# Kernel optimization log

Hardware: AMD Instinct MI355X
Metric: run time of the kernel (lower is better)

Reference implementation:

```python
import jax, jax.numpy as jnp
import numpy as np

H = 1536          # hidden_size
NUM_HEADS = 12
NUM_KV = 2
HEAD_DIM = 128
GQA_REP = NUM_HEADS // NUM_KV  # 6
MAX_CACHE = 131072
SCALE = HEAD_DIM ** -0.5


def setup_inputs() -> dict:
    key = jax.random.key(0)
    ks = jax.random.split(key, 8)
    w = 0.02  # weight init scale for numerical sanity
    return {
        "hidden_states": jax.random.normal(ks[0], (1, H, 1, 1), dtype=jnp.float32),
        "Wq": jax.random.normal(ks[1], (NUM_HEADS * HEAD_DIM, H), dtype=jnp.float32) * w,
        "Wk": jax.random.normal(ks[2], (NUM_KV * HEAD_DIM, H), dtype=jnp.float32) * w,
        "Wv": jax.random.normal(ks[3], (NUM_KV * HEAD_DIM, H), dtype=jnp.float32) * w,
        "Wo": jax.random.normal(ks[4], (H, NUM_HEADS * HEAD_DIM), dtype=jnp.float32) * w,
        "kv_cache_k": jax.random.normal(ks[5], (1, NUM_KV, MAX_CACHE, HEAD_DIM), dtype=jnp.float32),
        "kv_cache_v": jax.random.normal(ks[6], (1, NUM_KV, MAX_CACHE, HEAD_DIM), dtype=jnp.float32),
        "pos": MAX_CACHE - 1,  # python int: current cache write position
    }


def reference(hidden_states, Wq, Wk, Wv, Wo, kv_cache_k, kv_cache_v, pos):
    # 1x1 Conv2d on a [1,H,1,1] tensor == matvec.
    x = hidden_states.reshape(H)                      # [H]
    q = (Wq @ x).reshape(NUM_KV, GQA_REP, HEAD_DIM)   # [g, r, d]
    k = (Wk @ x).reshape(NUM_KV, 1, HEAD_DIM)         # [g, 1, d]
    v = (Wv @ x).reshape(NUM_KV, 1, HEAD_DIM)
    # in-place cache write at pos (pos < MAX_CACHE in this setup)
    kc = jax.lax.dynamic_update_slice(kv_cache_k[0], k, (0, pos, 0))  # [g, L, d]
    vc = jax.lax.dynamic_update_slice(kv_cache_v[0], v, (0, pos, 0))
    seq_len = min(pos + 1, MAX_CACHE)  # pos is a python int -> static slice
    kc = kc[:, :seq_len, :]
    vc = vc[:, :seq_len, :]
    # GQA without materializing repeated K/V: fold repeat into the q head axis.
    scores = jnp.einsum('grd,gld->grl', q, kc) * SCALE       # [g, r, L]
    attn = jax.nn.softmax(scores, axis=-1)
    out = jnp.einsum('grl,gld->grd', attn, vc)               # [g, r, d]
    y = Wo @ out.reshape(NUM_HEADS * HEAD_DIM)               # [H]
    return y.reshape(1, H, 1, 1)
```

## Files before the change

kernel.cpp:

```cpp
#include <hip/hip_runtime.h>
#include <math.h>

#define HDIM 1536
#define NUM_HEADS 12
#define NUM_KV 2
#define HEAD_DIM 128
#define GQA_REP 6
#define MAX_CACHE 131072
#define SCALE 0.08838834764831845f

#define WS_Q    0
#define WS_OUT  2048
#define WS_L2   4096
#define WS_PART 65536
#define REC 132

#define UNITS_PER_G 1024
#define NEG_BIG (-1.0e30f)
#define MASK_NEG (-1.0e38f)

__global__ __launch_bounds__(256) void proj_qkv(
    const float* __restrict__ x, const float* __restrict__ Wq,
    const float* __restrict__ Wk, const float* __restrict__ Wv,
    float* __restrict__ kv_k, float* __restrict__ kv_v,
    const int* __restrict__ pos_p, float* __restrict__ ws)
{
    int r    = (blockIdx.x * 256 + threadIdx.x) >> 6;
    int lane = threadIdx.x & 63;

    const float* Wrow;
    if (r < HDIM)            Wrow = Wq + (size_t)r * HDIM;
    else if (r < HDIM + 256) Wrow = Wk + (size_t)(r - HDIM) * HDIM;
    else                     Wrow = Wv + (size_t)(r - HDIM - 256) * HDIM;

    const float4* w4 = (const float4*)Wrow;
    const float4* x4 = (const float4*)x;
    float sum = 0.f;
#pragma unroll
    for (int it = 0; it < 6; ++it) {
        float4 a = w4[lane + 64 * it];
        float4 b = x4[lane + 64 * it];
        sum += a.x * b.x + a.y * b.y + a.z * b.z + a.w * b.w;
    }
#pragma unroll
    for (int off = 32; off >= 1; off >>= 1) sum += __shfl_xor(sum, off);

    if (lane == 0) {
        if (r < HDIM) {
            ws[WS_Q + r] = sum * SCALE;
        } else {
            int pos = *pos_p;
            if (r < HDIM + 256) {
                int j = r - HDIM; int g = j >> 7, d = j & 127;
                kv_k[((size_t)g * MAX_CACHE + pos) * HEAD_DIM + d] = sum;
            } else {
                int j = r - HDIM - 256; int g = j >> 7, d = j & 127;
                kv_v[((size_t)g * MAX_CACHE + pos) * HEAD_DIM + d] = sum;
            }
        }
    }
}

__global__ __launch_bounds__(256, 4) void attn_decode(
    const float* __restrict__ kv_k, const float* __restrict__ kv_v,
    const int* __restrict__ pos_p, float* __restrict__ ws)
{
    __shared__ float lds[4][GQA_REP][REC];

    int b    = blockIdx.x;
    int g    = b >> 10;
    int ublk = b & 1023;
    int wid  = threadIdx.x >> 6;
    int lane = threadIdx.x & 63;
    int h    = lane >> 5;
    int j    = lane & 31;

    int seq_len = *pos_p + 1;
    if (seq_len > MAX_CACHE) seq_len = MAX_CACHE;

    const float* qb = ws + WS_Q + g * (GQA_REP * HEAD_DIM);
    float4 q[GQA_REP];
#pragma unroll
    for (int r = 0; r < GQA_REP; ++r)
        q[r] = ((const float4*)(qb + r * HEAD_DIM))[j];

    float  m[GQA_REP], l[GQA_REP];
    float4 acc[GQA_REP];
#pragma unroll
    for (int r = 0; r < GQA_REP; ++r) {
        m[r] = NEG_BIG; l[r] = 0.f;
        acc[r].x = acc[r].y = acc[r].z = acc[r].w = 0.f;
    }

    int wbase = ublk * 128 + wid * 32;
    const float4* Kp = (const float4*)(kv_k + ((size_t)g * MAX_CACHE + wbase) * HEAD_DIM);
    const float4* Vp = (const float4*)(kv_v + ((size_t)g * MAX_CACHE + wbase) * HEAD_DIM);
    int i0 = h * 32 + j;

    float4 KA = Kp[i0],      KB = Kp[i0 + 64];
    float4 VA = Vp[i0],      VB = Vp[i0 + 64];

    for (int t = 0; t < 8; ++t) {
        float4 KAn, KBn, VAn, VBn;
        if (t < 7) {
            int n = i0 + (t + 1) * 128;
            KAn = Kp[n]; KBn = Kp[n + 64];
            VAn = Vp[n]; VBn = Vp[n + 64];
        }
        int pA = wbase + 4 * t + h;
        float maskA = (pA     < seq_len) ? 0.f : MASK_NEG;
        float maskB = (pA + 2 < seq_len) ? 0.f : MASK_NEG;

#pragma unroll
        for (int r = 0; r < GQA_REP; ++r) {
            float sA = KA.x * q[r].x + KA.y * q[r].y + KA.z * q[r].z + KA.w * q[r].w;
            float sB = KB.x * q[r].x + KB.y * q[r].y + KB.z * q[r].z + KB.w * q[r].w;
#pragma unroll
            for (int off = 16; off >= 1; off >>= 1) {
                sA += __shfl_xor(sA, off);
                sB += __shfl_xor(sB, off);
            }
            sA += maskA; sB += maskB;

            float mn    = fmaxf(m[r], fmaxf(sA, sB));
            float alpha = __expf(m[r] - mn);
            float pa    = __expf(sA - mn);
            float pb    = __expf(sB - mn);
            l[r] = l[r] * alpha + pa + pb;
            acc[r].x = acc[r].x * alpha + pa * VA.x + pb * VB.x;
            acc[r].y = acc[r].y * alpha + pa * VA.y + pb * VB.y;
            acc[r].z = acc[r].z * alpha + pa * VA.z + pb * VB.z;
            acc[r].w = acc[r].w * alpha + pa * VA.w + pb * VB.w;
            m[r] = mn;
        }
        KA = KAn; KB = KBn; VA = VAn; VB = VBn;
    }

#pragma unroll
    for (int r = 0; r < GQA_REP; ++r) {
        float mo = __shfl_xor(m[r], 32);
        float lo = __shfl_xor(l[r], 32);
        float4 ao;
        ao.x = __shfl_xor(acc[r].x, 32);
        ao.y = __shfl_xor(acc[r].y, 32);
        ao.z = __shfl_xor(acc[r].z, 32);
        ao.w = __shfl_xor(acc[r].w, 32);
        float M  = fmaxf(m[r], mo);
        float a0 = __expf(m[r] - M);
        float a1 = __expf(mo   - M);
        float L  = l[r] * a0 + lo * a1;
        float4 A;
        A.x = acc[r].x * a0 + ao.x * a1;
        A.y = acc[r].y * a0 + ao.y * a1;
        A.z = acc[r].z * a0 + ao.z * a1;
        A.w = acc[r].w * a0 + ao.w * a1;

        if (lane < 32) ((float4*)&lds[wid][r][4])[j] = A;
        if (lane == 0) { lds[wid][r][0] = M; lds[wid][r][1] = L; }
    }
    __syncthreads();

    for (int r = wid; r < GQA_REP; r += 4) {
        float m0 = lds[0][r][0], m1 = lds[1][r][0];
        float m2 = lds[2][r][0], m3 = lds[3][r][0];
        float M = fmaxf(fmaxf(m0, m1), fmaxf(m2, m3));
        float w0 = __expf(m0 - M), w1 = __expf(m1 - M);
        float w2 = __expf(m2 - M), w3 = __expf(m3 - M);
        float L = lds[0][r][1] * w0 + lds[1][r][1] * w1
                + lds[2][r][1] * w2 + lds[3][r][1] * w3;

        float2 a0v = ((const float2*)&lds[0][r][4])[lane];
        float2 a1v = ((const float2*)&lds[1][r][4])[lane];
        float2 a2v = ((const float2*)&lds[2][r][4])[lane];
        float2 a3v = ((const float2*)&lds[3][r][4])[lane];
        float2 a;
        a.x = a0v.x * w0 + a1v.x * w1 + a2v.x * w2 + a3v.x * w3;
        a.y = a0v.y * w0 + a1v.y * w1 + a2v.y * w2 + a3v.y * w3;

        float* rec = ws + WS_PART + ((size_t)(g * UNITS_PER_G + ublk) * GQA_REP + r) * REC;
        ((float2*)(rec + 4))[lane] = a;
        if (lane == 0) { rec[0] = M; rec[1] = L; }
    }
}

__global__ __launch_bounds__(64) void combine1(float* __restrict__ ws)
{
    int b  = blockIdx.x;
    int hh = b >> 5;
    int s  = b & 31;
    int g = hh / GQA_REP, r = hh % GQA_REP;
    int t  = threadIdx.x;
    int um = t & 31;

    const float* base = ws + WS_PART +
        ((size_t)(g * UNITS_PER_G + s * 32) * GQA_REP + r) * REC;
    const float* rec = base + (size_t)um * GQA_REP * REC;
    float mu = rec[0], lu = rec[1];

    float M = mu;
#pragma unroll
    for (int off = 16; off >= 1; off >>= 1) M = fmaxf(M, __shfl_xor(M, off));
    float w = __expf(mu - M);
    float L = lu * w;
#pragma unroll
    for (int off = 16; off >= 1; off >>= 1) L += __shfl_xor(L, off);

    float2 a; a.x = 0.f; a.y = 0.f;
    for (int uu = 0; uu < 32; ++uu) {
        float wu = __shfl(w, uu);
        float2 av = ((const float2*)(base + (size_t)uu * GQA_REP * REC + 4))[t];
        a.x += wu * av.x;
        a.y += wu * av.y;
    }
    float* orec = ws + WS_L2 + (size_t)(hh * 32 + s) * REC;
    ((float2*)(orec + 4))[t] = a;
    if (t == 0) { orec[0] = M; orec[1] = L; }
}

__global__ __launch_bounds__(64) void combine2(float* __restrict__ ws)
{
    int hh = blockIdx.x;
    int t  = threadIdx.x;
    int um = t & 31;

    const float* base = ws + WS_L2 + (size_t)(hh * 32) * REC;
    const float* rec  = base + (size_t)um * REC;
    float mu = rec[0], lu = rec[1];

    float M = mu;
#pragma unroll
    for (int off = 16; off >= 1; off >>= 1) M = fmaxf(M, __shfl_xor(M, off));
    float w = __expf(mu - M);
    float L = lu * w;
#pragma unroll
    for (int off = 16; off >= 1; off >>= 1) L += __shfl_xor(L, off);

    float2 a; a.x = 0.f; a.y = 0.f;
    for (int uu = 0; uu < 32; ++uu) {
        float wu = __shfl(w, uu);
        float2 av = ((const float2*)(base + (size_t)uu * REC + 4))[t];
        a.x += wu * av.x;
        a.y += wu * av.y;
    }
    float invL = 1.f / L;
    ws[WS_OUT + hh * HEAD_DIM + 2 * t]     = a.x * invL;
    ws[WS_OUT + hh * HEAD_DIM + 2 * t + 1] = a.y * invL;
}

__global__ __launch_bounds__(256) void proj_out(
    const float* __restrict__ Wo, const float* __restrict__ ws,
    float* __restrict__ y)
{
    int r    = (blockIdx.x * 256 + threadIdx.x) >> 6;
    int lane = threadIdx.x & 63;
    const float4* w4 = (const float4*)(Wo + (size_t)r * HDIM);
    const float4* o4 = (const float4*)(ws + WS_OUT);
    float sum = 0.f;
#pragma unroll
    for (int it = 0; it < 6; ++it) {
        float4 a = w4[lane + 64 * it];
        float4 b = o4[lane + 64 * it];
        sum += a.x * b.x + a.y * b.y + a.z * b.z + a.w * b.w;
    }
#pragma unroll
    for (int off = 32; off >= 1; off >>= 1) sum += __shfl_xor(sum, off);
    if (lane == 0) y[r] = sum;
}

extern "C" void kernel_launch(void* const* d_in, const int* in_sizes, int n_in,
                              void* d_out, int out_size, void* d_ws, size_t ws_size,
                              hipStream_t stream) {
    const float* x   = (const float*)d_in[0];
    const float* Wq  = (const float*)d_in[1];
    const float* Wk  = (const float*)d_in[2];
    const float* Wv  = (const float*)d_in[3];
    const float* Wo  = (const float*)d_in[4];
    float*       kvk = (float*)d_in[5];
    float*       kvv = (float*)d_in[6];
    const int*   pos = (const int*)d_in[7];
    float* ws = (float*)d_ws;
    float* y  = (float*)d_out;

    proj_qkv   <<<512,  256, 0, stream>>>(x, Wq, Wk, Wv, kvk, kvv, pos, ws);
    attn_decode<<<2048, 256, 0, stream>>>(kvk, kvv, pos, ws);
    combine1   <<<384,   64, 0, stream>>>(ws);
    combine2   <<< 12,   64, 0, stream>>>(ws);
    proj_out   <<<384,  256, 0, stream>>>(Wo, ws, y);
}
```

Measured before the change: 322.2 us.

## Stream KV tiles into double-buffered LDS via async global_load_lds

New measurement: 329.0 us. +2.1%, slower.

```diff
diff --git a/kernel.cpp b/kernel.cpp
--- a/kernel.cpp
+++ b/kernel.cpp
@@ -1,5 +1,6 @@
 #include <hip/hip_runtime.h>
 #include <math.h>
+#include <stdint.h>
 
 #define HDIM 1536
 #define NUM_HEADS 12
@@ -18,6 +19,9 @@
 #define UNITS_PER_G 1024
 #define NEG_BIG (-1.0e30f)
 #define MASK_NEG (-1.0e38f)
+
+#define GLOBAL_AS __attribute__((address_space(1)))
+#define LDS_AS    __attribute__((address_space(3)))
 
 __global__ __launch_bounds__(256) void proj_qkv(
     const float* __restrict__ x, const float* __restrict__ Wq,
@@ -65,7 +69,7 @@
     const float* __restrict__ kv_k, const float* __restrict__ kv_v,
     const int* __restrict__ pos_p, float* __restrict__ ws)
 {
-    __shared__ float lds[4][GQA_REP][REC];
+    __shared__ char smem[32768];
 
     int b    = blockIdx.x;
     int g    = b >> 10;
@@ -92,22 +96,43 @@
         acc[r].x = acc[r].y = acc[r].z = acc[r].w = 0.f;
     }
 
-    int wbase = ublk * 128 + wid * 32;
-    const float4* Kp = (const float4*)(kv_k + ((size_t)g * MAX_CACHE + wbase) * HEAD_DIM);
-    const float4* Vp = (const float4*)(kv_v + ((size_t)g * MAX_CACHE + wbase) * HEAD_DIM);
-    int i0 = h * 32 + j;
-
-    float4 KA = Kp[i0],      KB = Kp[i0 + 64];
-    float4 VA = Vp[i0],      VB = Vp[i0 + 64];
-
-    for (int t = 0; t < 8; ++t) {
-        float4 KAn, KBn, VAn, VBn;
-        if (t < 7) {
-            int n = i0 + (t + 1) * 128;
-            KAn = Kp[n]; KBn = Kp[n + 64];
-            VAn = Vp[n]; VBn = Vp[n + 64];
+    int blkbase = ublk * 128;
+    const float* Kg = kv_k + ((size_t)g * MAX_CACHE + blkbase) * HEAD_DIM;
+    const float* Vg = kv_v + ((size_t)g * MAX_CACHE + blkbase) * HEAD_DIM;
+
+    auto issue_stage = [&](int s) {
+        int parity = s & 1;
+#pragma unroll
+        for (int cc = 0; cc < 2; ++cc) {
+            int c = wid + 4 * cc;
+            int p0 = s * 16 + 2 * c;
+            const char* gk = (const char*)(Kg + (size_t)p0 * HEAD_DIM) + lane * 16;
+            const char* gv = (const char*)(Vg + (size_t)p0 * HEAD_DIM) + lane * 16;
+            char* lk = smem + parity * 16384 + c * 1024;
+            char* lv = smem + parity * 16384 + 8192 + c * 1024;
+            __builtin_amdgcn_global_load_lds((const GLOBAL_AS void*)gk,
+                                             (LDS_AS void*)lk, 16, 0, 0);
+            __builtin_amdgcn_global_load_lds((const GLOBAL_AS void*)gv,
+                                             (LDS_AS void*)lv, 16, 0, 0);
         }
-        int pA = wbase + 4 * t + h;
+    };
+
+    issue_stage(0);
+
+    for (int s = 0; s < 8; ++s) {
+        __syncthreads();
+        if (s < 7) issue_stage(s + 1);
+
+        int parity = s & 1;
+        int t0 = 4 * wid + h;
+        const float4* Kt = (const float4*)(smem + parity * 16384);
+        const float4* Vt = (const float4*)(smem + parity * 16384 + 8192);
+        float4 KA = Kt[t0 * 32 + j];
+        float4 KB = Kt[(t0 + 2) * 32 + j];
+        float4 VA = Vt[t0 * 32 + j];
+        float4 VB = Vt[(t0 + 2) * 32 + j];
+
+        int pA = blkbase + s * 16 + t0;
         float maskA = (pA     < seq_len) ? 0.f : MASK_NEG;
         float maskB = (pA + 2 < seq_len) ? 0.f : MASK_NEG;
 
@@ -133,9 +158,10 @@
             acc[r].w = acc[r].w * alpha + pa * VA.w + pb * VB.w;
             m[r] = mn;
         }
-        KA = KAn; KB = KBn; VA = VAn; VB = VBn;
-    }
-
+    }
+
+    __syncthreads();
+    float* mrg = (float*)smem;
 #pragma unroll
     for (int r = 0; r < GQA_REP; ++r) {
         float mo = __shfl_xor(m[r], 32);
@@ -155,24 +181,27 @@
         A.z = acc[r].z * a0 + ao.z * a1;
         A.w = acc[r].w * a0 + ao.w * a1;
 
-        if (lane < 32) ((float4*)&lds[wid][r][4])[j] = A;
-        if (lane == 0) { lds[wid][r][0] = M; lds[wid][r][1] = L; }
+        float* rr = mrg + ((size_t)wid * GQA_REP + r) * REC;
+        if (lane < 32) ((float4*)(rr + 4))[j] = A;
+        if (lane == 0) { rr[0] = M; rr[1] = L; }
     }
     __syncthreads();
 
     for (int r = wid; r < GQA_REP; r += 4) {
-        float m0 = lds[0][r][0], m1 = lds[1][r][0];
-        float m2 = lds[2][r][0], m3 = lds[3][r][0];
+        const float* r0 = mrg + (0 * GQA_REP + r) * REC;
+        const float* r1 = mrg + (1 * GQA_REP + r) * REC;
+        const float* r2 = mrg + (2 * GQA_REP + r) * REC;
+        const float* r3 = mrg + (3 * GQA_REP + r) * REC;
+        float m0 = r0[0], m1 = r1[0], m2 = r2[0], m3 = r3[0];
         float M = fmaxf(fmaxf(m0, m1), fmaxf(m2, m3));
         float w0 = __expf(m0 - M), w1 = __expf(m1 - M);
         float w2 = __expf(m2 - M), w3 = __expf(m3 - M);
-        float L = lds[0][r][1] * w0 + lds[1][r][1] * w1
-                + lds[2][r][1] * w2 + lds[3][r][1] * w3;
-
-        float2 a0v = ((const float2*)&lds[0][r][4])[lane];
-        float2 a1v = ((const float2*)&lds[1][r][4])[lane];
-        float2 a2v = ((const float2*)&lds[2][r][4])[lane];
-        float2 a3v = ((const float2*)&lds[3][r][4])[lane];
+        float L = r0[1] * w0 + r1[1] * w1 + r2[1] * w2 + r3[1] * w3;
+
+        float2 a0v = ((const float2*)(r0 + 4))[lane];
+        float2 a1v = ((const float2*)(r1 + 4))[lane];
+        float2 a2v = ((const float2*)(r2 + 4))[lane];
+        float2 a3v = ((const float2*)(r3 + 4))[lane];
         float2 a;
         a.x = a0v.x * w0 + a1v.x * w1 + a2v.x * w2 + a3v.x * w3;
         a.y = a0v.y * w0 + a1v.y * w1 + a2v.y * w2 + a3v.y * w3;
```
